# Kernel tuning notes

Measured on AMD Instinct MI355X. Metric: run time of the kernel, lower is better.

The kernel has to match this reference:

```python
import jax, jax.numpy as jnp
import numpy as np

B, L, T, TE, H = 16, 100, 50, 100, 200  # batch, post_len, triples/token, t_embed, hidden
NEG_INF = jnp.float32(-1e30)


def setup_inputs() -> dict:
    key = jax.random.key(0)
    ks = jax.random.split(key, 9)
    sc = 0.1
    inp = {
        'head_emb': jax.random.normal(ks[0], (B, L, T, TE), jnp.float32),
        'rel_emb':  jax.random.normal(ks[1], (B, L, T, TE), jnp.float32),
        'tail_emb': jax.random.normal(ks[2], (B, L, T, TE), jnp.float32),
        'Wh_w': jax.random.normal(ks[3], (H, TE), jnp.float32) * sc,
        'Wh_b': jax.random.normal(ks[4], (H,), jnp.float32) * sc,
        'Wr_w': jax.random.normal(ks[5], (H, TE), jnp.float32) * sc,
        'Wr_b': jax.random.normal(ks[6], (H,), jnp.float32) * sc,
        'Wt_w': jax.random.normal(ks[7], (H, TE), jnp.float32) * sc,
        'Wt_b': jax.random.normal(ks[8], (H,), jnp.float32) * sc,
    }
    # structured padding masks (like PAD_IDX padding): last quarter of triples padded,
    # last 10 post positions padded. Every unpadded post position has valid triples.
    inp['triple_mask'] = jnp.broadcast_to(jnp.arange(T) >= (3 * T) // 4, (B, L, T))
    inp['post_mask'] = jnp.broadcast_to(jnp.arange(L) >= L - 10, (B, L))
    return inp


def reference(head_emb, rel_emb, tail_emb, Wh_w, Wh_b, Wr_w, Wr_b, Wt_w, Wt_b,
              triple_mask, post_mask):
    # Linear projections: [B,L,T,TE] @ [TE,H] -> [B,L,T,H]
    h = jnp.einsum('bltd,hd->blth', head_emb, Wh_w) + Wh_b
    r = jnp.einsum('bltd,hd->blth', rel_emb, Wr_w) + Wr_b
    t = jnp.einsum('bltd,hd->blth', tail_emb, Wt_w) + Wt_b
    # triple-wise additive attention logit: [B,L,T]
    static_logit = jnp.sum(r * jnp.tanh(h + t), axis=-1)
    static_logit = jnp.where(triple_mask, NEG_INF, static_logit)
    static_logit = jnp.where(post_mask[:, :, None], 0.0, static_logit)
    static_attn = jax.nn.softmax(static_logit, axis=-1)  # [B,L,T]
    # weighted entity aggregation: ent = cat(head, tail) -> [B,L,2*TE]
    ent = jnp.concatenate([head_emb, tail_emb], axis=-1)
    static_graph = jnp.einsum('blte,blt->ble', ent, static_attn)
    return static_graph
```

## Files before the change

kernel.cpp:

```cpp
#include <hip/hip_runtime.h>
#include <math.h>

#define BB 16
#define LL 100
#define TT 50
#define TE 100
#define HH 200
#define NTL 13
#define NEG_INF_F (-1e30f)

typedef _Float16 fp16;
typedef fp16 half8 __attribute__((ext_vector_type(8)));
typedef float f32x4 __attribute__((ext_vector_type(4)));

#define MFMA16 __builtin_amdgcn_mfma_f32_16x16x32_f16

__global__ __launch_bounds__(256)
void wprep_kernel(const float* __restrict__ Wh, const float* __restrict__ Wr,
                  const float* __restrict__ Wt,
                  const float* __restrict__ Bh, const float* __restrict__ Br,
                  const float* __restrict__ Bt,
                  fp16* __restrict__ WB) {
    int idx = blockIdx.x * 256 + threadIdx.x;
    int elem = idx & 7;
    int lane = (idx >> 3) & 63;
    int ks   = (idx >> 9) & 3;
    int pn   = idx >> 11;
    int nt   = pn % NTL;
    int p    = pn / NTL;
    int k = ks * 32 + 8 * (lane >> 4) + elem;
    int n = nt * 16 + (lane & 15);
    const float* W = (p == 0) ? Wh : (p == 1) ? Wr : Wt;
    const float* Bi = (p == 0) ? Bh : (p == 1) ? Br : Bt;
    float v = 0.0f;
    if (n < HH) {
        if (k < TE)       v = W[n * TE + k];
        else if (k == TE) v = Bi[n];
    }
    WB[idx] = (fp16)v;
}

#define GATHER1(SRC, DST, RV)                                                   \
    {                                                                           \
        _Pragma("unroll")                                                       \
        for (int ks_ = 0; ks_ < 4; ++ks_) {                                     \
            f32x4 v0 = {0.f, 0.f, 0.f, 0.f}, v1 = {0.f, 0.f, 0.f, 0.f};         \
            float one_ = 0.f;                                                   \
            if (ks_ < 3) {                                                      \
                const int d0 = ks_ * 32 + 8 * lg;                               \
                if (RV) {                                                       \
                    v0 = *(const f32x4*)((SRC) + d0);                           \
                    v1 = *(const f32x4*)((SRC) + d0 + 4);                       \
                }                                                               \
            } else if ((RV) && lg == 0) {                                       \
                v0 = *(const f32x4*)((SRC) + 96);                               \
                one_ = 1.0f;                                                    \
            }                                                                   \
            half8 h8;                                                           \
            _Pragma("unroll")                                                   \
            for (int i_ = 0; i_ < 4; ++i_) {                                    \
                h8[i_]     = (fp16)v0[i_];                                      \
                h8[4 + i_] = (fp16)v1[i_];                                      \
            }                                                                   \
            if (ks_ == 3) h8[4] = (fp16)one_;            \
            DST[ks_] = h8;                                                      \
        }                                                                       \
    }

__global__ __launch_bounds__(128, 3)
void ccm_mfma_kernel(const float* __restrict__ head, const float* __restrict__ rel,
                     const float* __restrict__ tail,
                     const fp16* __restrict__ WB,
                     const int* __restrict__ tmask, const int* __restrict__ pmask,
                     float* __restrict__ out) {
    __shared__ float sscore[64];
    __shared__ float sattn[64];

    const int bl  = blockIdx.x;
    const int tid = threadIdx.x;
    const int wv  = tid >> 6;
    const int l   = tid & 63;
    const int lr  = l & 15;
    const int lg  = l >> 4;
    const int r0  = wv * 32 + lr;
    const int r1  = wv * 32 + 16 + lr;
    const bool rv0 = r0 < TT;
    const bool rv1 = r1 < TT;
    const size_t base0 = (size_t)bl * TT * TE;

    half8 H0[4], R0[4], T0[4], H1[4], R1[4], T1[4];
    GATHER1(head + base0 + (size_t)r0 * TE, H0, rv0);
    GATHER1(rel  + base0 + (size_t)r0 * TE, R0, rv0);
    GATHER1(tail + base0 + (size_t)r0 * TE, T0, rv0);
    GATHER1(head + base0 + (size_t)r1 * TE, H1, rv1);
    GATHER1(rel  + base0 + (size_t)r1 * TE, R1, rv1);
    GATHER1(tail + base0 + (size_t)r1 * TE, T1, rv1);

    float sc0[4] = {0.f, 0.f, 0.f, 0.f};
    float sc1[4] = {0.f, 0.f, 0.f, 0.f};
    const int ps = NTL * 4 * 64 * 8;

    #pragma unroll 1
    for (int nt = 0; nt < NTL; ++nt) {
        f32x4 aH0 = {0,0,0,0}, aR0 = {0,0,0,0}, aT0 = {0,0,0,0};
        f32x4 aH1 = {0,0,0,0}, aR1 = {0,0,0,0}, aT1 = {0,0,0,0};
        const int ob0 = nt * 2048 + l * 8;
        #pragma unroll
        for (int ks = 0; ks < 4; ++ks) {
            const int ob = ob0 + ks * 512;
            half8 wH = *(const half8*)(WB + ob);
            half8 wR = *(const half8*)(WB + ps + ob);
            half8 wT = *(const half8*)(WB + 2 * ps + ob);
            aH0 = MFMA16(H0[ks], wH, aH0, 0, 0, 0);
            aH1 = MFMA16(H1[ks], wH, aH1, 0, 0, 0);
            aR0 = MFMA16(R0[ks], wR, aR0, 0, 0, 0);
            aR1 = MFMA16(R1[ks], wR, aR1, 0, 0, 0);
            aT0 = MFMA16(T0[ks], wT, aT0, 0, 0, 0);
            aT1 = MFMA16(T1[ks], wT, aT1, 0, 0, 0);
        }
        #pragma unroll
        for (int g = 0; g < 4; ++g) {
            float s0 = aH0[g] + aT0[g];
            float e0 = __expf(2.f * s0);
            float t0 = 1.f - 2.f / (e0 + 1.f);
            sc0[g] = fmaf(aR0[g], t0, sc0[g]);
            float s1 = aH1[g] + aT1[g];
            float e1 = __expf(2.f * s1);
            float t1 = 1.f - 2.f / (e1 + 1.f);
            sc1[g] = fmaf(aR1[g], t1, sc1[g]);
        }
    }

    #pragma unroll
    for (int g = 0; g < 4; ++g) {
        float s = sc0[g];
        s += __shfl_xor(s, 1); s += __shfl_xor(s, 2);
        s += __shfl_xor(s, 4); s += __shfl_xor(s, 8);
        const int tr = wv * 32 + lg * 4 + g;
        if (lr == 0 && tr < TT) sscore[tr] = s;
        float s1 = sc1[g];
        s1 += __shfl_xor(s1, 1); s1 += __shfl_xor(s1, 2);
        s1 += __shfl_xor(s1, 4); s1 += __shfl_xor(s1, 8);
        const int tr1 = wv * 32 + 16 + lg * 4 + g;
        if (lr == 0 && tr1 < TT) sscore[tr1] = s1;
    }
    __syncthreads();

    if (tid < 64) {
        const int t = tid;
        const bool valid = t < TT;
        float lgt = valid ? sscore[t] : 0.f;
        const bool tm = valid ? (tmask[bl * TT + t] != 0) : false;
        const bool pm = pmask[bl] != 0;
        float logit = pm ? 0.f : (tm ? NEG_INF_F : lgt);
        float mx = valid ? logit : -3.0e38f;
        #pragma unroll
        for (int o = 32; o; o >>= 1) mx = fmaxf(mx, __shfl_xor(mx, o));
        float e = valid ? __expf(logit - mx) : 0.f;
        float s = e;
        #pragma unroll
        for (int o = 32; o; o >>= 1) s += __shfl_xor(s, o);
        if (valid) sattn[t] = e / s;
    }
    __syncthreads();

    for (int e = tid; e < 2 * TE; e += 128) {
        const float* src = (e < TE ? head + base0 + e
                                   : tail + base0 + (e - TE));
        float acc = 0.f;
        #pragma unroll
        for (int t = 0; t < TT; ++t) acc = fmaf(src[t * TE], sattn[t], acc);
        out[(size_t)bl * (2 * TE) + e] = acc;
    }
}

extern "C" void kernel_launch(void* const* d_in, const int* in_sizes, int n_in,
                              void* d_out, int out_size, void* d_ws, size_t ws_size,
                              hipStream_t stream) {
    const float* head = (const float*)d_in[0];
    const float* rel  = (const float*)d_in[1];
    const float* tail = (const float*)d_in[2];
    const float* Whw  = (const float*)d_in[3];
    const float* Whb  = (const float*)d_in[4];
    const float* Wrw  = (const float*)d_in[5];
    const float* Wrb  = (const float*)d_in[6];
    const float* Wtw  = (const float*)d_in[7];
    const float* Wtb  = (const float*)d_in[8];
    const int* tmask  = (const int*)d_in[9];
    const int* pmask  = (const int*)d_in[10];
    float* out = (float*)d_out;

    fp16* WB = (fp16*)d_ws;

    wprep_kernel<<<(3 * NTL * 2048) / 256, 256, 0, stream>>>(Whw, Wrw, Wtw,
                                                             Whb, Wrb, Wtb, WB);
    ccm_mfma_kernel<<<BB * LL, 128, 0, stream>>>(head, rel, tail, WB,
                                                 tmask, pmask, out);
}
```

Before: 186.2 us.

## Stage weight tiles in LDS with double-buffered async loads, two rows per block

Weight layout is reordered so the H/R/T slices for each N-tile sit contiguously. These slices are then streamed into double-buffered shared memory with global_load_lds while the previous tile's MFMAs run. Each block now handles two (b,l) rows with 256 threads, so one weight staging is shared by two rows, and the softmax and aggregation phases are extended to match. The cost is two barriers per tile iteration and about 24KB of LDS per block, which may limit occupancy.

Result: faster. 179.0 us (-3.9%).

```diff
diff --git a/kernel.cpp b/kernel.cpp
--- a/kernel.cpp
+++ b/kernel.cpp
@@ -25,12 +25,12 @@
     int elem = idx & 7;
     int lane = (idx >> 3) & 63;
     int ks   = (idx >> 9) & 3;
-    int pn   = idx >> 11;
-    int nt   = pn % NTL;
-    int p    = pn / NTL;
+    int np   = idx >> 11;
+    int p    = np % 3;
+    int nt   = np / 3;
     int k = ks * 32 + 8 * (lane >> 4) + elem;
     int n = nt * 16 + (lane & 15);
-    const float* W = (p == 0) ? Wh : (p == 1) ? Wr : Wt;
+    const float* W  = (p == 0) ? Wh : (p == 1) ? Wr : Wt;
     const float* Bi = (p == 0) ? Bh : (p == 1) ? Br : Bt;
     float v = 0.0f;
     if (n < HH) {
@@ -67,23 +67,40 @@
         }                                                                       \
     }
 
-__global__ __launch_bounds__(128, 3)
+#define STAGE3(GBASE, LBASE)                                                    \
+    {                                                                           \
+        _Pragma("unroll")                                                       \
+        for (int u_ = 0; u_ < 3; ++u_) {                                        \
+            const int unit_ = wv * 3 + u_;                                      \
+            __builtin_amdgcn_global_load_lds(                                   \
+                (const __attribute__((address_space(1))) unsigned int*)         \
+                    ((GBASE) + unit_ * 512 + l * 8),                            \
+                (__attribute__((address_space(3))) unsigned int*)               \
+                    ((LBASE) + unit_ * 512),                                    \
+                16, 0, 0);                                                      \
+        }                                                                       \
+    }
+
+__global__ __launch_bounds__(256, 3)
 void ccm_mfma_kernel(const float* __restrict__ head, const float* __restrict__ rel,
                      const float* __restrict__ tail,
                      const fp16* __restrict__ WB,
                      const int* __restrict__ tmask, const int* __restrict__ pmask,
                      float* __restrict__ out) {
-    __shared__ float sscore[64];
-    __shared__ float sattn[64];
-
-    const int bl  = blockIdx.x;
+    __shared__ fp16 sw[2][6144];
+    __shared__ float sscore[2][64];
+    __shared__ float sattn[2][64];
+
     const int tid = threadIdx.x;
     const int wv  = tid >> 6;
     const int l   = tid & 63;
     const int lr  = l & 15;
     const int lg  = l >> 4;
-    const int r0  = wv * 32 + lr;
-    const int r1  = wv * 32 + 16 + lr;
+    const int blx = wv >> 1;
+    const int wp  = wv & 1;
+    const int bl  = 2 * blockIdx.x + blx;
+    const int r0  = wp * 32 + lr;
+    const int r1  = wp * 32 + 16 + lr;
     const bool rv0 = r0 < TT;
     const bool rv1 = r1 < TT;
     const size_t base0 = (size_t)bl * TT * TE;
@@ -96,21 +113,32 @@
     GATHER1(rel  + base0 + (size_t)r1 * TE, R1, rv1);
     GATHER1(tail + base0 + (size_t)r1 * TE, T1, rv1);
 
+    STAGE3(WB, &sw[0][0]);
+
     float sc0[4] = {0.f, 0.f, 0.f, 0.f};
     float sc1[4] = {0.f, 0.f, 0.f, 0.f};
-    const int ps = NTL * 4 * 64 * 8;
 
     #pragma unroll 1
     for (int nt = 0; nt < NTL; ++nt) {
+        const int cur = nt & 1;
+        if (nt + 1 < NTL) {
+            STAGE3(WB + (size_t)(nt + 1) * 6144, &sw[cur ^ 1][0]);
+            __builtin_amdgcn_sched_barrier(0);
+            asm volatile("s_waitcnt vmcnt(3)" ::: "memory");
+        } else {
+            __builtin_amdgcn_sched_barrier(0);
+            asm volatile("s_waitcnt vmcnt(0)" ::: "memory");
+        }
+        __syncthreads();
+
+        const fp16* wbuf = (const fp16*)&sw[cur][0];
         f32x4 aH0 = {0,0,0,0}, aR0 = {0,0,0,0}, aT0 = {0,0,0,0};
         f32x4 aH1 = {0,0,0,0}, aR1 = {0,0,0,0}, aT1 = {0,0,0,0};
-        const int ob0 = nt * 2048 + l * 8;
         #pragma unroll
         for (int ks = 0; ks < 4; ++ks) {
-            const int ob = ob0 + ks * 512;
-            half8 wH = *(const half8*)(WB + ob);
-            half8 wR = *(const half8*)(WB + ps + ob);
-            half8 wT = *(const half8*)(WB + 2 * ps + ob);
+            half8 wH = *(const half8*)(wbuf + (0 * 4 + ks) * 512 + l * 8);
+            half8 wR = *(const half8*)(wbuf + (1 * 4 + ks) * 512 + l * 8);
+            half8 wT = *(const half8*)(wbuf + (2 * 4 + ks) * 512 + l * 8);
             aH0 = MFMA16(H0[ks], wH, aH0, 0, 0, 0);
             aH1 = MFMA16(H1[ks], wH, aH1, 0, 0, 0);
             aR0 = MFMA16(R0[ks], wR, aR0, 0, 0, 0);
@@ -129,6 +157,7 @@
             float t1 = 1.f - 2.f / (e1 + 1.f);
             sc1[g] = fmaf(aR1[g], t1, sc1[g]);
         }
+        __syncthreads();
     }
 
     #pragma unroll
@@ -136,22 +165,24 @@
         float s = sc0[g];
         s += __shfl_xor(s, 1); s += __shfl_xor(s, 2);
         s += __shfl_xor(s, 4); s += __shfl_xor(s, 8);
-        const int tr = wv * 32 + lg * 4 + g;
-        if (lr == 0 && tr < TT) sscore[tr] = s;
+        const int tr = wp * 32 + lg * 4 + g;
+        if (lr == 0 && tr < TT) sscore[blx][tr] = s;
         float s1 = sc1[g];
         s1 += __shfl_xor(s1, 1); s1 += __shfl_xor(s1, 2);
         s1 += __shfl_xor(s1, 4); s1 += __shfl_xor(s1, 8);
-        const int tr1 = wv * 32 + 16 + lg * 4 + g;
-        if (lr == 0 && tr1 < TT) sscore[tr1] = s1;
+        const int tr1 = wp * 32 + 16 + lg * 4 + g;
+        if (lr == 0 && tr1 < TT) sscore[blx][tr1] = s1;
     }
     __syncthreads();
 
-    if (tid < 64) {
-        const int t = tid;
+    if (tid < 128) {
+        const int bx = tid >> 6;
+        const int t  = tid & 63;
+        const int mybl = 2 * blockIdx.x + bx;
         const bool valid = t < TT;
-        float lgt = valid ? sscore[t] : 0.f;
-        const bool tm = valid ? (tmask[bl * TT + t] != 0) : false;
-        const bool pm = pmask[bl] != 0;
+        float lgt = valid ? sscore[bx][t] : 0.f;
+        const bool tm = valid ? (tmask[mybl * TT + t] != 0) : false;
+        const bool pm = pmask[mybl] != 0;
         float logit = pm ? 0.f : (tm ? NEG_INF_F : lgt);
         float mx = valid ? logit : -3.0e38f;
         #pragma unroll
@@ -160,17 +191,23 @@
         float s = e;
         #pragma unroll
         for (int o = 32; o; o >>= 1) s += __shfl_xor(s, o);
-        if (valid) sattn[t] = e / s;
+        if (valid) sattn[bx][t] = e / s;
     }
     __syncthreads();
 
-    for (int e = tid; e < 2 * TE; e += 128) {
-        const float* src = (e < TE ? head + base0 + e
-                                   : tail + base0 + (e - TE));
-        float acc = 0.f;
-        #pragma unroll
-        for (int t = 0; t < TT; ++t) acc = fmaf(src[t * TE], sattn[t], acc);
-        out[(size_t)bl * (2 * TE) + e] = acc;
+    #pragma unroll
+    for (int it = 0; it < 2; ++it) {
+        const int i = tid + it * 256;
+        if (i < 2 * (2 * TE)) {
+            const int bx = (i >= 2 * TE) ? 1 : 0;
+            const int e  = i - bx * (2 * TE);
+            const size_t b2 = (size_t)(2 * blockIdx.x + bx) * TT * TE;
+            const float* src = (e < TE) ? head + b2 + e : tail + b2 + (e - TE);
+            float acc = 0.f;
+            #pragma unroll
+            for (int t = 0; t < TT; ++t) acc = fmaf(src[t * TE], sattn[bx][t], acc);
+            out[(size_t)(2 * blockIdx.x + bx) * (2 * TE) + e] = acc;
+        }
     }
 }
 
@@ -192,8 +229,8 @@
 
     fp16* WB = (fp16*)d_ws;
 
-    wprep_kernel<<<(3 * NTL * 2048) / 256, 256, 0, stream>>>(Whw, Wrw, Wtw,
+    wprep_kernel<<<(NTL * 3 * 2048) / 256, 256, 0, stream>>>(Whw, Wrw, Wtw,
                                                              Whb, Wrb, Wtb, WB);
-    ccm_mfma_kernel<<<BB * LL, 128, 0, stream>>>(head, rel, tail, WB,
-                                                 tmask, pmask, out);
+    ccm_mfma_kernel<<<(BB * LL) / 2, 256, 0, stream>>>(head, rel, tail, WB,
+                                                       tmask, pmask, out);
 }
```
